# Performance work log

Measured on AMD Instinct MI355X. Metric: run time of the kernel, lower is better.

## Reference

```python
import jax, jax.numpy as jnp
import numpy as np

HIDDEN = 2048
HEADS = 16
HEAD_DIM = HIDDEN // HEADS  # 128
NUM_LATENTS = 16
LN_EPS = 1e-5


def setup_inputs() -> dict:
    key = jax.random.key(0)
    ks = jax.random.split(key, 16)
    B, S, D = 8, 4096, HIDDEN
    glorot = lambda k, fi, fo: jax.random.uniform(k, (fi, fo), jnp.float32,
                                                  -np.sqrt(6.0 / (fi + fo)), np.sqrt(6.0 / (fi + fo)))
    return {
        "hidden_states": jax.random.normal(ks[0], (B, S, D), jnp.float32),
        "ln_g": jnp.ones((D,), jnp.float32),
        "ln_b": jnp.zeros((D,), jnp.float32),
        "latents": 0.02 * jax.random.normal(ks[1], (NUM_LATENTS, D), jnp.float32),
        # weights stored as [in, out] (transpose of torch Linear.weight)
        "w_lq": glorot(ks[2], D, D), "b_lq": jnp.zeros((D,), jnp.float32),
        "w_k": glorot(ks[3], D, D), "b_k": jnp.zeros((D,), jnp.float32),
        "w_v": glorot(ks[4], D, D), "b_v": jnp.zeros((D,), jnp.float32),
        "w_lv": glorot(ks[5], D, D), "b_lv": jnp.zeros((D,), jnp.float32),
        "w_out": glorot(ks[6], D, D), "b_out": jnp.zeros((D,), jnp.float32),
    }


def reference(hidden_states, ln_g, ln_b, latents, w_lq, b_lq, w_k, b_k,
              w_v, b_v, w_lv, b_lv, w_out, b_out):
    x = hidden_states
    B, S, D = x.shape
    H, hd, L = HEADS, HEAD_DIM, latents.shape[0]
    # pre-LayerNorm
    mu = jnp.mean(x, axis=-1, keepdims=True)
    var = jnp.var(x, axis=-1, keepdims=True)
    h = (x - mu) / jnp.sqrt(var + LN_EPS) * ln_g + ln_b
    # projections
    k = (h @ w_k + b_k).reshape(B, S, H, hd)          # keys   [B,S,H,hd]
    v = (h @ w_v + b_v).reshape(B, S, H, hd)          # values [B,S,H,hd]
    q = (latents @ w_lq + b_lq).reshape(L, H, hd)     # latent queries [L,H,hd]
    # latent cross-attention: scores [B,H,L,S]
    scores = jnp.einsum("lhd,bshd->bhls", q, k) / np.sqrt(hd).astype(x.dtype)
    probs = jax.nn.softmax(scores, axis=-1)           # dropout is identity at eval
    ctx = jnp.einsum("bhls,bshd->blhd", probs, v).reshape(B, L, D)
    lv = ctx @ w_lv + b_lv                            # [B,L,D]
    pooled = jnp.mean(lv, axis=1, keepdims=True)      # [B,1,D]
    out = pooled @ w_out + b_out                      # [B,1,D]
    return x + jnp.broadcast_to(out, (B, S, D))       # residual add
```

## Files before the change

kernel.cpp:

```cpp
#include <hip/hip_runtime.h>
#include <hip/hip_bf16.h>

#define BB 8
#define SS 4096
#define DD 2048
#define HH 16
#define HDIM 128
#define LL 16
#define JJ 256
#define ROWS (BB*SS)
#define LN_EPS 1e-5f

typedef __attribute__((ext_vector_type(8))) short short8;
typedef __attribute__((ext_vector_type(4))) float f32x4;

typedef __attribute__((address_space(1))) const unsigned int gu32;
typedef __attribute__((address_space(3))) unsigned int lu32;
__device__ __forceinline__ void async16(const void* g, void* l) {
  __builtin_amdgcn_global_load_lds((gu32*)g, (lu32*)l, 16, 0, 0);
}

__device__ __forceinline__ unsigned short f2bf(float f) {
  unsigned int u = __builtin_bit_cast(unsigned int, f);
  u += 0x7fffu + ((u >> 16) & 1u);
  return (unsigned short)(u >> 16);
}
__device__ __forceinline__ float bf2f(unsigned short u) {
  unsigned int v = ((unsigned int)u) << 16;
  return __builtin_bit_cast(float, v);
}

__global__ __launch_bounds__(256) void k_q_part(const float* latents, const float* w_lq, float* qpart) {
  int c  = blockIdx.x * 256 + threadIdx.x;
  int e0 = blockIdx.y * 64;
  float acc[16];
#pragma unroll
  for (int l = 0; l < 16; ++l) acc[l] = 0.f;
  for (int e = e0; e < e0 + 64; ++e) {
    float w = w_lq[(size_t)e * 2048 + c];
#pragma unroll
    for (int l = 0; l < 16; ++l) acc[l] += latents[l * 2048 + e] * w;
  }
#pragma unroll
  for (int l = 0; l < 16; ++l) qpart[((size_t)blockIdx.y * 16 + l) * 2048 + c] = acc[l];
}

__global__ __launch_bounds__(256) void k_reduce(const float* part, const float* bias, float* out, int R) {
  int c = blockIdx.x * 256 + threadIdx.x;
  int r = blockIdx.y;
  float s = bias[c];
  for (int p = 0; p < 32; ++p) s += part[((size_t)p * R + r) * 2048 + c];
  out[r * 2048 + c] = s;
}

__global__ __launch_bounds__(256) void k_lnT(const float* x, const float* ln_g, const float* ln_b,
                                             short* h) {
  int row = blockIdx.x;
  int t = threadIdx.x;
  const float4* xr = (const float4*)(x + (size_t)row * 2048);
  float4 v0 = xr[t * 2];
  float4 v1 = xr[t * 2 + 1];
  float s  = v0.x + v0.y + v0.z + v0.w + v1.x + v1.y + v1.z + v1.w;
  float s2 = v0.x*v0.x + v0.y*v0.y + v0.z*v0.z + v0.w*v0.w
           + v1.x*v1.x + v1.y*v1.y + v1.z*v1.z + v1.w*v1.w;
#pragma unroll
  for (int o = 32; o; o >>= 1) { s += __shfl_down(s, o); s2 += __shfl_down(s2, o); }
  __shared__ float red[8];
  int wid = t >> 6;
  if ((t & 63) == 0) { red[wid] = s; red[4 + wid] = s2; }
  __syncthreads();
  float ts  = red[0] + red[1] + red[2] + red[3];
  float ts2 = red[4] + red[5] + red[6] + red[7];
  float mu   = ts * (1.0f / 2048.0f);
  float var  = ts2 * (1.0f / 2048.0f) - mu * mu;
  float rstd = rsqrtf(var + LN_EPS);
  const float4* gp = (const float4*)ln_g;
  const float4* bp = (const float4*)ln_b;
  float4 g0 = gp[t * 2], g1 = gp[t * 2 + 1];
  float4 b0 = bp[t * 2], b1 = bp[t * 2 + 1];
  short8 o;
  o[0] = (short)f2bf((v0.x - mu) * rstd * g0.x + b0.x);
  o[1] = (short)f2bf((v0.y - mu) * rstd * g0.y + b0.y);
  o[2] = (short)f2bf((v0.z - mu) * rstd * g0.z + b0.z);
  o[3] = (short)f2bf((v0.w - mu) * rstd * g0.w + b0.w);
  o[4] = (short)f2bf((v1.x - mu) * rstd * g1.x + b1.x);
  o[5] = (short)f2bf((v1.y - mu) * rstd * g1.y + b1.y);
  o[6] = (short)f2bf((v1.z - mu) * rstd * g1.z + b1.z);
  o[7] = (short)f2bf((v1.w - mu) * rstd * g1.w + b1.w);
  ((short8*)(h + (size_t)row * 2048))[t] = o;
}

__global__ __launch_bounds__(256) void k_wq(const float* w_k, const float* q, short* wq_t) {
  int e = blockIdx.x;
  __shared__ float wrow[2048];
  for (int i = threadIdx.x; i < 512; i += 256)
    ((float4*)wrow)[i] = ((const float4*)(w_k + (size_t)e * 2048))[i];
  __syncthreads();
  int j = threadIdx.x;
  int h = j >> 4, l = j & 15;
  const float* qrow = q + l * 2048 + h * 128;
  const float* wr = wrow + h * 128;
  float acc = 0.f;
#pragma unroll 8
  for (int d = 0; d < 128; ++d) acc += wr[d] * qrow[d];
  wq_t[(size_t)j * 2048 + e] = (short)f2bf(acc * 0.08838834764831845f);
}

__global__ __launch_bounds__(256, 2) void k_scores(const short* h, const short* wq_t,
                                                   short* scores, float* part_ms) {
  int s0 = blockIdx.x * 256;
  int j0 = blockIdx.y * 64;
  int b  = blockIdx.z;
  __shared__ short lds[2 * 4096 + 2 * 16384];
  int t = threadIdx.x, lane = t & 63, w = t >> 6;
  f32x4 zero = {0.f, 0.f, 0.f, 0.f};
  f32x4 acc[4][4];
#pragma unroll
  for (int m = 0; m < 4; ++m)
#pragma unroll
    for (int n = 0; n < 4; ++n) acc[m][n] = zero;

  int rsel = t >> 3;
  int kcs  = (t & 7) ^ ((t >> 3) & 7);
  const short* hbase  = h + ((size_t)(b * 4096 + s0)) * 2048;
  const short* wqbase = wq_t + (size_t)j0 * 2048;
  int koff0 = (((lane >> 4)) ^ (lane & 7)) * 8;
  int koff1 = ((4 + (lane >> 4)) ^ (lane & 7)) * 8;

  int cur = 0;
  {
    short* lA = lds;
    short* lB = lds + 8192;
#pragma unroll
    for (int i = 0; i < 8; ++i)
      async16(hbase + (size_t)(i * 32 + rsel) * 2048 + kcs * 8,
              lB + (i * 256 + w * 64) * 8);
#pragma unroll
    for (int i = 0; i < 2; ++i)
      async16(wqbase + (size_t)(i * 32 + rsel) * 2048 + kcs * 8,
              lA + (i * 256 + w * 64) * 8);
  }

  for (int it = 0; it < 32; ++it) {
    if (it < 31) {
      int k0 = (it + 1) * 64;
      short* lA1 = lds + (cur ^ 1) * 4096;
      short* lB1 = lds + 8192 + (cur ^ 1) * 16384;
#pragma unroll
      for (int i = 0; i < 8; ++i)
        async16(hbase + (size_t)(i * 32 + rsel) * 2048 + k0 + kcs * 8,
                lB1 + (i * 256 + w * 64) * 8);
#pragma unroll
      for (int i = 0; i < 2; ++i)
        async16(wqbase + (size_t)(i * 32 + rsel) * 2048 + k0 + kcs * 8,
                lA1 + (i * 256 + w * 64) * 8);
      asm volatile("s_waitcnt vmcnt(10)" ::: "memory");
    } else {
      asm volatile("s_waitcnt vmcnt(0)" ::: "memory");
    }
    __builtin_amdgcn_s_barrier();
    __builtin_amdgcn_sched_barrier(0);
    const short* lA = lds + cur * 4096;
    const short* lB = lds + 8192 + cur * 16384;
#pragma unroll
    for (int kk = 0; kk < 2; ++kk) {
      int ko = kk ? koff1 : koff0;
      short8 afr[4];
#pragma unroll
      for (int m = 0; m < 4; ++m)
        afr[m] = *(const short8*)(lA + (m * 16 + (lane & 15)) * 64 + ko);
#pragma unroll
      for (int n = 0; n < 4; ++n) {
        short8 bfr = *(const short8*)(lB + (w * 64 + n * 16 + (lane & 15)) * 64 + ko);
#pragma unroll
        for (int m = 0; m < 4; ++m)
          acc[m][n] = __builtin_amdgcn_mfma_f32_16x16x32_bf16(afr[m], bfr, acc[m][n], 0, 0, 0);
      }
    }
    __builtin_amdgcn_s_barrier();
    cur ^= 1;
  }

  int hi = lane >> 4, cc = lane & 15;
  __syncthreads();
  float2* msred = (float2*)lds;
#pragma unroll
  for (int m = 0; m < 4; ++m) {
#pragma unroll
    for (int i = 0; i < 4; ++i) {
      int j = j0 + m * 16 + hi * 4 + i;
      float v[4];
#pragma unroll
      for (int n = 0; n < 4; ++n) {
        unsigned short u = f2bf(acc[m][n][i]);
        scores[((size_t)(b * 256 + j)) * 4096 + s0 + w * 64 + n * 16 + cc] = (short)u;
        v[n] = bf2f(u);
      }
      float mx = fmaxf(fmaxf(v[0], v[1]), fmaxf(v[2], v[3]));
#pragma unroll
      for (int o = 1; o < 16; o <<= 1) mx = fmaxf(mx, __shfl_xor(mx, o));
      float sm = __expf(v[0] - mx) + __expf(v[1] - mx) + __expf(v[2] - mx) + __expf(v[3] - mx);
#pragma unroll
      for (int o = 1; o < 16; o <<= 1) sm += __shfl_xor(sm, o);
      if (cc == 0) msred[(m * 16 + hi * 4 + i) * 4 + w] = make_float2(mx, sm);
    }
  }
  __syncthreads();
  if (t < 64) {
    float2 p0 = msred[t * 4 + 0], p1 = msred[t * 4 + 1];
    float2 p2 = msred[t * 4 + 2], p3 = msred[t * 4 + 3];
    float M = fmaxf(fmaxf(p0.x, p1.x), fmaxf(p2.x, p3.x));
    float S = p0.y * __expf(p0.x - M) + p1.y * __expf(p1.x - M)
            + p2.y * __expf(p2.x - M) + p3.y * __expf(p3.x - M);
    ((float2*)part_ms)[((size_t)(b * 256 + j0 + t)) * 16 + blockIdx.x] = make_float2(M, S);
  }
}

__global__ __launch_bounds__(256) void k_pt(const short* scores, const float* part_ms,
                                            const short* h, float* Tpart) {
  int sp = blockIdx.x;
  int b  = blockIdx.y;
  int t  = threadIdx.x;
  __shared__ short sc[256 * 128];
  __shared__ float lp[16 * 128];
  __shared__ float lms[512];
  {
    const float2* p = ((const float2*)part_ms) + (size_t)(b * 256 + t) * 16;
    float2 v[16];
    float M = -1e30f;
#pragma unroll
    for (int i = 0; i < 16; ++i) { v[i] = p[i]; M = fmaxf(M, v[i].x); }
    float S = 0.f;
#pragma unroll
    for (int i = 0; i < 16; ++i) S += v[i].y * __expf(v[i].x - M);
    lms[t * 2] = M; lms[t * 2 + 1] = 1.0f / (16.0f * S);
  }
#pragma unroll
  for (int rr = 0; rr < 2; ++rr) {
    int j = rr * 128 + (t >> 1);
    const short8* src = (const short8*)(scores + ((size_t)(b * 256 + j)) * 4096 + sp * 128 + (t & 1) * 64);
    short8* dst = (short8*)(sc + j * 128 + (t & 1) * 64);
#pragma unroll
    for (int i = 0; i < 8; ++i) dst[i] = src[i];
  }
  __syncthreads();
  {
    int s = t & 127, hg = (t >> 7) * 8;
    for (int hh = hg; hh < hg + 8; ++hh) {
      float accp = 0.f;
#pragma unroll
      for (int l = 0; l < 16; ++l) {
        int r = hh * 16 + l;
        accp += __expf(bf2f((unsigned short)sc[r * 128 + s]) - lms[r * 2]) * lms[r * 2 + 1];
      }
      lp[hh * 128 + s] = accp;
    }
  }
  __syncthreads();
  f32x4 a0[16], a1[16];
#pragma unroll
  for (int hh = 0; hh < 16; ++hh) { a0[hh] = (f32x4){0,0,0,0}; a1[hh] = (f32x4){0,0,0,0}; }
  const short* hb = h + ((size_t)(b * 4096 + sp * 128)) * 2048 + t * 8;
  for (int si = 0; si < 128; ++si) {
    short8 hv8 = *(const short8*)(hb + (size_t)si * 2048);
    float hv[8];
#pragma unroll
    for (int c = 0; c < 8; ++c) hv[c] = bf2f((unsigned short)hv8[c]);
#pragma unroll
    for (int hh = 0; hh < 16; ++hh) {
      float p = lp[hh * 128 + si];
#pragma unroll
      for (int c = 0; c < 4; ++c) { a0[hh][c] += p * hv[c]; a1[hh][c] += p * hv[4 + c]; }
    }
  }
#pragma unroll
  for (int hh = 0; hh < 16; ++hh) {
    float* dst = Tpart + ((size_t)(sp * 128 + b * 16 + hh)) * 2048 + t * 8;
    *(f32x4*)dst = a0[hh];
    *(f32x4*)(dst + 4) = a1[hh];
  }
}

__global__ __launch_bounds__(256) void k_cbar_part(const float* Tpart, const float* w_v, float* part) {
  int t  = threadIdx.x;
  int c  = blockIdx.x * 256 + t;
  int e0 = blockIdx.y * 64;
  __shared__ float tb[2][8][64];
  {
    int idx = t * 4;
    int hl = idx >> 9, b = (idx >> 6) & 7, ee = idx & 63;
    int hg = blockIdx.x * 2 + hl;
    f32x4 s = {0.f, 0.f, 0.f, 0.f};
    for (int sp = 0; sp < 32; ++sp) {
      f32x4 v = *(const f32x4*)(Tpart + ((size_t)(sp * 128 + b * 16 + hg)) * 2048 + e0 + ee);
      s += v;
    }
    *(f32x4*)&tb[hl][b][ee] = s;
  }
  __syncthreads();
  int h1 = t >> 7;
  float acc[8];
#pragma unroll
  for (int b = 0; b < 8; ++b) acc[b] = 0.f;
  for (int e = 0; e < 64; ++e) {
    float wv = w_v[(size_t)(e0 + e) * 2048 + c];
#pragma unroll
    for (int b = 0; b < 8; ++b) acc[b] += tb[h1][b][e] * wv;
  }
#pragma unroll
  for (int b = 0; b < 8; ++b) part[((size_t)blockIdx.y * 8 + b) * 2048 + c] = acc[b];
}

__global__ __launch_bounds__(256) void k_vecmat_part(const float* partin, const float* bias,
                                                     const float* W, float* partout) {
  int t  = threadIdx.x;
  int c  = blockIdx.x * 256 + t;
  int e0 = blockIdx.y * 64;
  __shared__ float vin[8][64];
  {
#pragma unroll
    for (int k = 0; k < 2; ++k) {
      int idx = t * 2 + k;
      int b = idx >> 6, ee = idx & 63;
      float s = bias[e0 + ee];
      for (int p = 0; p < 32; ++p) s += partin[((size_t)p * 8 + b) * 2048 + e0 + ee];
      vin[b][ee] = s;
    }
  }
  __syncthreads();
  float acc[8];
#pragma unroll
  for (int b = 0; b < 8; ++b) acc[b] = 0.f;
  for (int e = 0; e < 64; ++e) {
    float wv = W[(size_t)(e0 + e) * 2048 + c];
#pragma unroll
    for (int b = 0; b < 8; ++b) acc[b] += vin[b][e] * wv;
  }
#pragma unroll
  for (int b = 0; b < 8; ++b) partout[((size_t)blockIdx.y * 8 + b) * 2048 + c] = acc[b];
}

__global__ __launch_bounds__(256) void k_resid(const float* x, const float* outv, float* out) {
  size_t i4 = (size_t)blockIdx.x * 256 + threadIdx.x;
  size_t total4 = (size_t)ROWS * 512;
  size_t stride = (size_t)gridDim.x * 256;
  for (; i4 < total4; i4 += stride) {
    int b  = (int)(i4 >> 21);
    int c4 = (int)(i4 & 511);
    float4 xv = ((const float4*)x)[i4];
    float4 ov = ((const float4*)outv)[b * 512 + c4];
    float4 o;
    o.x = xv.x + ov.x; o.y = xv.y + ov.y;
    o.z = xv.z + ov.z; o.w = xv.w + ov.w;
    ((float4*)out)[i4] = o;
  }
}

extern "C" void kernel_launch(void* const* d_in, const int* in_sizes, int n_in,
                              void* d_out, int out_size, void* d_ws, size_t ws_size,
                              hipStream_t stream) {
  const float* x       = (const float*)d_in[0];
  const float* ln_g    = (const float*)d_in[1];
  const float* ln_b    = (const float*)d_in[2];
  const float* latents = (const float*)d_in[3];
  const float* w_lq    = (const float*)d_in[4];
  const float* b_lq    = (const float*)d_in[5];
  const float* w_k     = (const float*)d_in[6];
  const float* w_v     = (const float*)d_in[8];
  const float* b_v     = (const float*)d_in[9];
  const float* w_lv    = (const float*)d_in[10];
  const float* b_lv    = (const float*)d_in[11];
  const float* w_out   = (const float*)d_in[12];
  const float* b_out   = (const float*)d_in[13];

  char* base = (char*)d_out;
  short* scores  = (short*)(base);
  short* h       = (short*)(base + 16777216);
  float* Tpart   = (float*)(base + 150994944);
  float* part_ms = (float*)(base + 184549376);
  float* q       = (float*)(base + 184811520);
  short* wq_t    = (short*)(base + 184942592);
  float* qpart   = (float*)(base + 185991168);
  float* part    = (float*)(base + 190185472);
  float* part2   = (float*)(base + 192282624);
  float* outv    = (float*)d_ws;
  float* out     = (float*)d_out;

  k_q_part     <<<dim3(8, 32), 256, 0, stream>>>(latents, w_lq, qpart);
  k_reduce     <<<dim3(8, 16), 256, 0, stream>>>(qpart, b_lq, q, 16);
  k_lnT        <<<32768, 256, 0, stream>>>(x, ln_g, ln_b, h);
  k_wq         <<<2048, 256, 0, stream>>>(w_k, q, wq_t);
  k_scores     <<<dim3(16, 4, 8), 256, 0, stream>>>(h, wq_t, scores, part_ms);
  k_pt         <<<dim3(32, 8), 256, 0, stream>>>(scores, part_ms, h, Tpart);
  k_cbar_part  <<<dim3(8, 32), 256, 0, stream>>>(Tpart, w_v, part);
  k_vecmat_part<<<dim3(8, 32), 256, 0, stream>>>(part, b_v, w_lv, part2);
  k_vecmat_part<<<dim3(8, 32), 256, 0, stream>>>(part2, b_lv, w_out, part);
  k_reduce     <<<dim3(8, 8), 256, 0, stream>>>(part, b_out, outv, 8);
  k_resid      <<<2048, 256, 0, stream>>>(x, outv, out);
}
```

Measured before the change: 429.3 us.

## Halve score tile width, triple-buffer loads, and split k_pt across feature halves

Measured after the change: 421.3 us, median of 2. Within noise of the previous version (-1.9%).

```diff
diff --git a/kernel.cpp b/kernel.cpp
--- a/kernel.cpp
+++ b/kernel.cpp
@@ -108,17 +108,17 @@
 
 __global__ __launch_bounds__(256, 2) void k_scores(const short* h, const short* wq_t,
                                                    short* scores, float* part_ms) {
-  int s0 = blockIdx.x * 256;
+  int s0 = blockIdx.x * 128;
   int j0 = blockIdx.y * 64;
   int b  = blockIdx.z;
-  __shared__ short lds[2 * 4096 + 2 * 16384];
+  __shared__ short lds[3 * 12288];
   int t = threadIdx.x, lane = t & 63, w = t >> 6;
   f32x4 zero = {0.f, 0.f, 0.f, 0.f};
-  f32x4 acc[4][4];
+  f32x4 acc[4][2];
 #pragma unroll
   for (int m = 0; m < 4; ++m)
 #pragma unroll
-    for (int n = 0; n < 4; ++n) acc[m][n] = zero;
+    for (int n = 0; n < 2; ++n) acc[m][n] = zero;
 
   int rsel = t >> 3;
   int kcs  = (t & 7) ^ ((t >> 3) & 7);
@@ -127,41 +127,34 @@
   int koff0 = (((lane >> 4)) ^ (lane & 7)) * 8;
   int koff1 = ((4 + (lane >> 4)) ^ (lane & 7)) * 8;
 
-  int cur = 0;
-  {
-    short* lA = lds;
-    short* lB = lds + 8192;
-#pragma unroll
-    for (int i = 0; i < 8; ++i)
-      async16(hbase + (size_t)(i * 32 + rsel) * 2048 + kcs * 8,
-              lB + (i * 256 + w * 64) * 8);
-#pragma unroll
-    for (int i = 0; i < 2; ++i)
-      async16(wqbase + (size_t)(i * 32 + rsel) * 2048 + kcs * 8,
-              lA + (i * 256 + w * 64) * 8);
-  }
-
+#define STAGE_SC(IT, BUF) { \
+    int k0_ = (IT) * 64; \
+    short* lA_ = lds + (BUF) * 12288; \
+    short* lB_ = lA_ + 4096; \
+    _Pragma("unroll") \
+    for (int i_ = 0; i_ < 4; ++i_) \
+      async16(hbase + (size_t)(i_ * 32 + rsel) * 2048 + k0_ + kcs * 8, lB_ + (i_ * 256 + t) * 8); \
+    _Pragma("unroll") \
+    for (int i_ = 0; i_ < 2; ++i_) \
+      async16(wqbase + (size_t)(i_ * 32 + rsel) * 2048 + k0_ + kcs * 8, lA_ + (i_ * 256 + t) * 8); \
+  }
+
+  STAGE_SC(0, 0);
+  STAGE_SC(1, 1);
+  int cb = 0, sb = 2;
   for (int it = 0; it < 32; ++it) {
-    if (it < 31) {
-      int k0 = (it + 1) * 64;
-      short* lA1 = lds + (cur ^ 1) * 4096;
-      short* lB1 = lds + 8192 + (cur ^ 1) * 16384;
-#pragma unroll
-      for (int i = 0; i < 8; ++i)
-        async16(hbase + (size_t)(i * 32 + rsel) * 2048 + k0 + kcs * 8,
-                lB1 + (i * 256 + w * 64) * 8);
-#pragma unroll
-      for (int i = 0; i < 2; ++i)
-        async16(wqbase + (size_t)(i * 32 + rsel) * 2048 + k0 + kcs * 8,
-                lA1 + (i * 256 + w * 64) * 8);
-      asm volatile("s_waitcnt vmcnt(10)" ::: "memory");
+    if (it < 30) {
+      STAGE_SC(it + 2, sb);
+      asm volatile("s_waitcnt vmcnt(12)" ::: "memory");
+    } else if (it == 30) {
+      asm volatile("s_waitcnt vmcnt(6)" ::: "memory");
     } else {
       asm volatile("s_waitcnt vmcnt(0)" ::: "memory");
     }
     __builtin_amdgcn_s_barrier();
     __builtin_amdgcn_sched_barrier(0);
-    const short* lA = lds + cur * 4096;
-    const short* lB = lds + 8192 + cur * 16384;
+    const short* lA = lds + cb * 12288;
+    const short* lB = lA + 4096;
 #pragma unroll
     for (int kk = 0; kk < 2; ++kk) {
       int ko = kk ? koff1 : koff0;
@@ -170,16 +163,18 @@
       for (int m = 0; m < 4; ++m)
         afr[m] = *(const short8*)(lA + (m * 16 + (lane & 15)) * 64 + ko);
 #pragma unroll
-      for (int n = 0; n < 4; ++n) {
-        short8 bfr = *(const short8*)(lB + (w * 64 + n * 16 + (lane & 15)) * 64 + ko);
+      for (int n = 0; n < 2; ++n) {
+        short8 bfr = *(const short8*)(lB + (w * 32 + n * 16 + (lane & 15)) * 64 + ko);
 #pragma unroll
         for (int m = 0; m < 4; ++m)
           acc[m][n] = __builtin_amdgcn_mfma_f32_16x16x32_bf16(afr[m], bfr, acc[m][n], 0, 0, 0);
       }
     }
     __builtin_amdgcn_s_barrier();
-    cur ^= 1;
-  }
+    cb = (cb == 2) ? 0 : cb + 1;
+    sb = (sb == 2) ? 0 : sb + 1;
+  }
+#undef STAGE_SC
 
   int hi = lane >> 4, cc = lane & 15;
   __syncthreads();
@@ -189,17 +184,17 @@
 #pragma unroll
     for (int i = 0; i < 4; ++i) {
       int j = j0 + m * 16 + hi * 4 + i;
-      float v[4];
-#pragma unroll
-      for (int n = 0; n < 4; ++n) {
+      float v[2];
+#pragma unroll
+      for (int n = 0; n < 2; ++n) {
         unsigned short u = f2bf(acc[m][n][i]);
-        scores[((size_t)(b * 256 + j)) * 4096 + s0 + w * 64 + n * 16 + cc] = (short)u;
+        scores[((size_t)(b * 256 + j)) * 4096 + s0 + w * 32 + n * 16 + cc] = (short)u;
         v[n] = bf2f(u);
       }
-      float mx = fmaxf(fmaxf(v[0], v[1]), fmaxf(v[2], v[3]));
+      float mx = fmaxf(v[0], v[1]);
 #pragma unroll
       for (int o = 1; o < 16; o <<= 1) mx = fmaxf(mx, __shfl_xor(mx, o));
-      float sm = __expf(v[0] - mx) + __expf(v[1] - mx) + __expf(v[2] - mx) + __expf(v[3] - mx);
+      float sm = __expf(v[0] - mx) + __expf(v[1] - mx);
 #pragma unroll
       for (int o = 1; o < 16; o <<= 1) sm += __shfl_xor(sm, o);
       if (cc == 0) msred[(m * 16 + hi * 4 + i) * 4 + w] = make_float2(mx, sm);
@@ -212,7 +207,7 @@
     float M = fmaxf(fmaxf(p0.x, p1.x), fmaxf(p2.x, p3.x));
     float S = p0.y * __expf(p0.x - M) + p1.y * __expf(p1.x - M)
             + p2.y * __expf(p2.x - M) + p3.y * __expf(p3.x - M);
-    ((float2*)part_ms)[((size_t)(b * 256 + j0 + t)) * 16 + blockIdx.x] = make_float2(M, S);
+    ((float2*)part_ms)[((size_t)(b * 256 + j0 + t)) * 32 + blockIdx.x] = make_float2(M, S);
   }
 }
 
@@ -220,19 +215,19 @@
                                             const short* h, float* Tpart) {
   int sp = blockIdx.x;
   int b  = blockIdx.y;
+  int eh = blockIdx.z;
   int t  = threadIdx.x;
   __shared__ short sc[256 * 128];
   __shared__ float lp[16 * 128];
   __shared__ float lms[512];
   {
-    const float2* p = ((const float2*)part_ms) + (size_t)(b * 256 + t) * 16;
-    float2 v[16];
+    const float2* p = ((const float2*)part_ms) + (size_t)(b * 256 + t) * 32;
     float M = -1e30f;
 #pragma unroll
-    for (int i = 0; i < 16; ++i) { v[i] = p[i]; M = fmaxf(M, v[i].x); }
+    for (int i = 0; i < 32; ++i) M = fmaxf(M, p[i].x);
     float S = 0.f;
 #pragma unroll
-    for (int i = 0; i < 16; ++i) S += v[i].y * __expf(v[i].x - M);
+    for (int i = 0; i < 32; ++i) S += p[i].y * __expf(p[i].x - M);
     lms[t * 2] = M; lms[t * 2 + 1] = 1.0f / (16.0f * S);
   }
 #pragma unroll
@@ -257,28 +252,26 @@
     }
   }
   __syncthreads();
-  f32x4 a0[16], a1[16];
-#pragma unroll
-  for (int hh = 0; hh < 16; ++hh) { a0[hh] = (f32x4){0,0,0,0}; a1[hh] = (f32x4){0,0,0,0}; }
-  const short* hb = h + ((size_t)(b * 4096 + sp * 128)) * 2048 + t * 8;
+  f32x4 a[16];
+#pragma unroll
+  for (int hh = 0; hh < 16; ++hh) a[hh] = (f32x4){0.f, 0.f, 0.f, 0.f};
+  int e0 = eh * 1024 + t * 4;
+  const short* hb = h + ((size_t)(b * 4096 + sp * 128)) * 2048 + e0;
   for (int si = 0; si < 128; ++si) {
-    short8 hv8 = *(const short8*)(hb + (size_t)si * 2048);
-    float hv[8];
-#pragma unroll
-    for (int c = 0; c < 8; ++c) hv[c] = bf2f((unsigned short)hv8[c]);
+    short4 hv4 = *(const short4*)(hb + (size_t)si * 2048);
+    float hv[4];
+    hv[0] = bf2f((unsigned short)hv4.x); hv[1] = bf2f((unsigned short)hv4.y);
+    hv[2] = bf2f((unsigned short)hv4.z); hv[3] = bf2f((unsigned short)hv4.w);
 #pragma unroll
     for (int hh = 0; hh < 16; ++hh) {
       float p = lp[hh * 128 + si];
 #pragma unroll
-      for (int c = 0; c < 4; ++c) { a0[hh][c] += p * hv[c]; a1[hh][c] += p * hv[4 + c]; }
-    }
-  }
-#pragma unroll
-  for (int hh = 0; hh < 16; ++hh) {
-    float* dst = Tpart + ((size_t)(sp * 128 + b * 16 + hh)) * 2048 + t * 8;
-    *(f32x4*)dst = a0[hh];
-    *(f32x4*)(dst + 4) = a1[hh];
-  }
+      for (int c = 0; c < 4; ++c) a[hh][c] += p * hv[c];
+    }
+  }
+#pragma unroll
+  for (int hh = 0; hh < 16; ++hh)
+    *(f32x4*)(Tpart + ((size_t)(sp * 128 + b * 16 + hh)) * 2048 + e0) = a[hh];
 }
 
 __global__ __launch_bounds__(256) void k_cbar_part(const float* Tpart, const float* w_v, float* part) {
@@ -378,11 +371,11 @@
   short* h       = (short*)(base + 16777216);
   float* Tpart   = (float*)(base + 150994944);
   float* part_ms = (float*)(base + 184549376);
-  float* q       = (float*)(base + 184811520);
-  short* wq_t    = (short*)(base + 184942592);
-  float* qpart   = (float*)(base + 185991168);
-  float* part    = (float*)(base + 190185472);
-  float* part2   = (float*)(base + 192282624);
+  float* q       = (float*)(base + 185073664);
+  short* wq_t    = (short*)(base + 185204736);
+  float* qpart   = (float*)(base + 186253312);
+  float* part    = (float*)(base + 190447616);
+  float* part2   = (float*)(base + 192544768);
   float* outv    = (float*)d_ws;
   float* out     = (float*)d_out;
 
@@ -390,8 +383,8 @@
   k_reduce     <<<dim3(8, 16), 256, 0, stream>>>(qpart, b_lq, q, 16);
   k_lnT        <<<32768, 256, 0, stream>>>(x, ln_g, ln_b, h);
   k_wq         <<<2048, 256, 0, stream>>>(w_k, q, wq_t);
-  k_scores     <<<dim3(16, 4, 8), 256, 0, stream>>>(h, wq_t, scores, part_ms);
-  k_pt         <<<dim3(32, 8), 256, 0, stream>>>(scores, part_ms, h, Tpart);
+  k_scores     <<<dim3(32, 4, 8), 256, 0, stream>>>(h, wq_t, scores, part_ms);
+  k_pt         <<<dim3(32, 8, 2), 256, 0, stream>>>(scores, part_ms, h, Tpart);
   k_cbar_part  <<<dim3(8, 32), 256, 0, stream>>>(Tpart, w_v, part);
   k_vecmat_part<<<dim3(8, 32), 256, 0, stream>>>(part, b_v, w_lv, part2);
   k_vecmat_part<<<dim3(8, 32), 256, 0, stream>>>(part2, b_lv, w_out, part);
```

## Retile scores GEMM over all 256 query columns and split PT across feature halves

Applied to the files above, without the earlier changes.

New measurement: 424.7 us. No clear change (-1.1%).

```diff
diff --git a/kernel.cpp b/kernel.cpp
--- a/kernel.cpp
+++ b/kernel.cpp
@@ -108,10 +108,9 @@
 
 __global__ __launch_bounds__(256, 2) void k_scores(const short* h, const short* wq_t,
                                                    short* scores, float* part_ms) {
-  int s0 = blockIdx.x * 256;
-  int j0 = blockIdx.y * 64;
-  int b  = blockIdx.z;
-  __shared__ short lds[2 * 4096 + 2 * 16384];
+  int s0 = blockIdx.x * 64;
+  int b  = blockIdx.y;
+  __shared__ short lds[2 * 16384 + 2 * 4096];
   int t = threadIdx.x, lane = t & 63, w = t >> 6;
   f32x4 zero = {0.f, 0.f, 0.f, 0.f};
   f32x4 acc[4][4];
@@ -120,58 +119,57 @@
 #pragma unroll
     for (int n = 0; n < 4; ++n) acc[m][n] = zero;
 
-  int rsel = t >> 3;
-  int kcs  = (t & 7) ^ ((t >> 3) & 7);
-  const short* hbase  = h + ((size_t)(b * 4096 + s0)) * 2048;
-  const short* wqbase = wq_t + (size_t)j0 * 2048;
+  int jlo = w * 8 + (lane >> 3);
+  int kcs = (lane & 7) ^ ((lane >> 3) & 7);
+  const short* hbase = h + ((size_t)(b * 4096 + s0)) * 2048;
   int koff0 = (((lane >> 4)) ^ (lane & 7)) * 8;
   int koff1 = ((4 + (lane >> 4)) ^ (lane & 7)) * 8;
 
   int cur = 0;
   {
     short* lA = lds;
-    short* lB = lds + 8192;
+    short* lB = lds + 32768;
 #pragma unroll
     for (int i = 0; i < 8; ++i)
-      async16(hbase + (size_t)(i * 32 + rsel) * 2048 + kcs * 8,
+      async16(wq_t + (size_t)(i * 32 + jlo) * 2048 + kcs * 8,
+              lA + (i * 256 + w * 64) * 8);
+#pragma unroll
+    for (int i = 0; i < 2; ++i)
+      async16(hbase + (size_t)(i * 32 + jlo) * 2048 + kcs * 8,
               lB + (i * 256 + w * 64) * 8);
-#pragma unroll
-    for (int i = 0; i < 2; ++i)
-      async16(wqbase + (size_t)(i * 32 + rsel) * 2048 + kcs * 8,
-              lA + (i * 256 + w * 64) * 8);
   }
 
   for (int it = 0; it < 32; ++it) {
     if (it < 31) {
       int k0 = (it + 1) * 64;
-      short* lA1 = lds + (cur ^ 1) * 4096;
-      short* lB1 = lds + 8192 + (cur ^ 1) * 16384;
+      short* lA1 = lds + (cur ^ 1) * 16384;
+      short* lB1 = lds + 32768 + (cur ^ 1) * 4096;
 #pragma unroll
       for (int i = 0; i < 8; ++i)
-        async16(hbase + (size_t)(i * 32 + rsel) * 2048 + k0 + kcs * 8,
+        async16(wq_t + (size_t)(i * 32 + jlo) * 2048 + k0 + kcs * 8,
+                lA1 + (i * 256 + w * 64) * 8);
+#pragma unroll
+      for (int i = 0; i < 2; ++i)
+        async16(hbase + (size_t)(i * 32 + jlo) * 2048 + k0 + kcs * 8,
                 lB1 + (i * 256 + w * 64) * 8);
-#pragma unroll
-      for (int i = 0; i < 2; ++i)
-        async16(wqbase + (size_t)(i * 32 + rsel) * 2048 + k0 + kcs * 8,
-                lA1 + (i * 256 + w * 64) * 8);
       asm volatile("s_waitcnt vmcnt(10)" ::: "memory");
     } else {
       asm volatile("s_waitcnt vmcnt(0)" ::: "memory");
     }
     __builtin_amdgcn_s_barrier();
     __builtin_amdgcn_sched_barrier(0);
-    const short* lA = lds + cur * 4096;
-    const short* lB = lds + 8192 + cur * 16384;
+    const short* lA = lds + cur * 16384;
+    const short* lB = lds + 32768 + cur * 4096;
 #pragma unroll
     for (int kk = 0; kk < 2; ++kk) {
       int ko = kk ? koff1 : koff0;
       short8 afr[4];
 #pragma unroll
       for (int m = 0; m < 4; ++m)
-        afr[m] = *(const short8*)(lA + (m * 16 + (lane & 15)) * 64 + ko);
+        afr[m] = *(const short8*)(lA + (w * 64 + m * 16 + (lane & 15)) * 64 + ko);
 #pragma unroll
       for (int n = 0; n < 4; ++n) {
-        short8 bfr = *(const short8*)(lB + (w * 64 + n * 16 + (lane & 15)) * 64 + ko);
+        short8 bfr = *(const short8*)(lB + (n * 16 + (lane & 15)) * 64 + ko);
 #pragma unroll
         for (int m = 0; m < 4; ++m)
           acc[m][n] = __builtin_amdgcn_mfma_f32_16x16x32_bf16(afr[m], bfr, acc[m][n], 0, 0, 0);
@@ -182,18 +180,16 @@
   }
 
   int hi = lane >> 4, cc = lane & 15;
-  __syncthreads();
-  float2* msred = (float2*)lds;
 #pragma unroll
   for (int m = 0; m < 4; ++m) {
 #pragma unroll
     for (int i = 0; i < 4; ++i) {
-      int j = j0 + m * 16 + hi * 4 + i;
+      int j = w * 64 + m * 16 + hi * 4 + i;
       float v[4];
 #pragma unroll
       for (int n = 0; n < 4; ++n) {
         unsigned short u = f2bf(acc[m][n][i]);
-        scores[((size_t)(b * 256 + j)) * 4096 + s0 + w * 64 + n * 16 + cc] = (short)u;
+        scores[((size_t)(b * 256 + j)) * 4096 + s0 + n * 16 + cc] = (short)u;
         v[n] = bf2f(u);
       }
       float mx = fmaxf(fmaxf(v[0], v[1]), fmaxf(v[2], v[3]));
@@ -202,17 +198,9 @@
       float sm = __expf(v[0] - mx) + __expf(v[1] - mx) + __expf(v[2] - mx) + __expf(v[3] - mx);
 #pragma unroll
       for (int o = 1; o < 16; o <<= 1) sm += __shfl_xor(sm, o);
-      if (cc == 0) msred[(m * 16 + hi * 4 + i) * 4 + w] = make_float2(mx, sm);
-    }
-  }
-  __syncthreads();
-  if (t < 64) {
-    float2 p0 = msred[t * 4 + 0], p1 = msred[t * 4 + 1];
-    float2 p2 = msred[t * 4 + 2], p3 = msred[t * 4 + 3];
-    float M = fmaxf(fmaxf(p0.x, p1.x), fmaxf(p2.x, p3.x));
-    float S = p0.y * __expf(p0.x - M) + p1.y * __expf(p1.x - M)
-            + p2.y * __expf(p2.x - M) + p3.y * __expf(p3.x - M);
-    ((float2*)part_ms)[((size_t)(b * 256 + j0 + t)) * 16 + blockIdx.x] = make_float2(M, S);
+      if (cc == 0)
+        ((float2*)part_ms)[((size_t)(b * 256 + j)) * 64 + blockIdx.x] = make_float2(mx, sm);
+    }
   }
 }
 
@@ -220,19 +208,19 @@
                                             const short* h, float* Tpart) {
   int sp = blockIdx.x;
   int b  = blockIdx.y;
+  int eh = blockIdx.z;
   int t  = threadIdx.x;
   __shared__ short sc[256 * 128];
   __shared__ float lp[16 * 128];
   __shared__ float lms[512];
   {
-    const float2* p = ((const float2*)part_ms) + (size_t)(b * 256 + t) * 16;
-    float2 v[16];
+    const float2* p = ((const float2*)part_ms) + (size_t)(b * 256 + t) * 64;
     float M = -1e30f;
-#pragma unroll
-    for (int i = 0; i < 16; ++i) { v[i] = p[i]; M = fmaxf(M, v[i].x); }
+#pragma unroll 8
+    for (int i = 0; i < 64; ++i) M = fmaxf(M, p[i].x);
     float S = 0.f;
-#pragma unroll
-    for (int i = 0; i < 16; ++i) S += v[i].y * __expf(v[i].x - M);
+#pragma unroll 8
+    for (int i = 0; i < 64; ++i) S += p[i].y * __expf(p[i].x - M);
     lms[t * 2] = M; lms[t * 2 + 1] = 1.0f / (16.0f * S);
   }
 #pragma unroll
@@ -257,28 +245,26 @@
     }
   }
   __syncthreads();
-  f32x4 a0[16], a1[16];
-#pragma unroll
-  for (int hh = 0; hh < 16; ++hh) { a0[hh] = (f32x4){0,0,0,0}; a1[hh] = (f32x4){0,0,0,0}; }
-  const short* hb = h + ((size_t)(b * 4096 + sp * 128)) * 2048 + t * 8;
+  f32x4 a[16];
+#pragma unroll
+  for (int hh = 0; hh < 16; ++hh) a[hh] = (f32x4){0.f, 0.f, 0.f, 0.f};
+  int e0 = eh * 1024 + t * 4;
+  const short* hb = h + ((size_t)(b * 4096 + sp * 128)) * 2048 + e0;
   for (int si = 0; si < 128; ++si) {
-    short8 hv8 = *(const short8*)(hb + (size_t)si * 2048);
-    float hv[8];
-#pragma unroll
-    for (int c = 0; c < 8; ++c) hv[c] = bf2f((unsigned short)hv8[c]);
+    short4 hv4 = *(const short4*)(hb + (size_t)si * 2048);
+    float hv[4];
+    hv[0] = bf2f((unsigned short)hv4.x); hv[1] = bf2f((unsigned short)hv4.y);
+    hv[2] = bf2f((unsigned short)hv4.z); hv[3] = bf2f((unsigned short)hv4.w);
 #pragma unroll
     for (int hh = 0; hh < 16; ++hh) {
       float p = lp[hh * 128 + si];
 #pragma unroll
-      for (int c = 0; c < 4; ++c) { a0[hh][c] += p * hv[c]; a1[hh][c] += p * hv[4 + c]; }
-    }
-  }
-#pragma unroll
-  for (int hh = 0; hh < 16; ++hh) {
-    float* dst = Tpart + ((size_t)(sp * 128 + b * 16 + hh)) * 2048 + t * 8;
-    *(f32x4*)dst = a0[hh];
-    *(f32x4*)(dst + 4) = a1[hh];
-  }
+      for (int c = 0; c < 4; ++c) a[hh][c] += p * hv[c];
+    }
+  }
+#pragma unroll
+  for (int hh = 0; hh < 16; ++hh)
+    *(f32x4*)(Tpart + ((size_t)(sp * 128 + b * 16 + hh)) * 2048 + e0) = a[hh];
 }
 
 __global__ __launch_bounds__(256) void k_cbar_part(const float* Tpart, const float* w_v, float* part) {
@@ -378,11 +364,11 @@
   short* h       = (short*)(base + 16777216);
   float* Tpart   = (float*)(base + 150994944);
   float* part_ms = (float*)(base + 184549376);
-  float* q       = (float*)(base + 184811520);
-  short* wq_t    = (short*)(base + 184942592);
-  float* qpart   = (float*)(base + 185991168);
-  float* part    = (float*)(base + 190185472);
-  float* part2   = (float*)(base + 192282624);
+  float* q       = (float*)(base + 185597952);
+  short* wq_t    = (short*)(base + 185729024);
+  float* qpart   = (float*)(base + 186777600);
+  float* part    = (float*)(base + 190971904);
+  float* part2   = (float*)(base + 193069056);
   float* outv    = (float*)d_ws;
   float* out     = (float*)d_out;
 
@@ -390,8 +376,8 @@
   k_reduce     <<<dim3(8, 16), 256, 0, stream>>>(qpart, b_lq, q, 16);
   k_lnT        <<<32768, 256, 0, stream>>>(x, ln_g, ln_b, h);
   k_wq         <<<2048, 256, 0, stream>>>(w_k, q, wq_t);
-  k_scores     <<<dim3(16, 4, 8), 256, 0, stream>>>(h, wq_t, scores, part_ms);
-  k_pt         <<<dim3(32, 8), 256, 0, stream>>>(scores, part_ms, h, Tpart);
+  k_scores     <<<dim3(64, 8), 256, 0, stream>>>(h, wq_t, scores, part_ms);
+  k_pt         <<<dim3(32, 8, 2), 256, 0, stream>>>(scores, part_ms, h, Tpart);
   k_cbar_part  <<<dim3(8, 32), 256, 0, stream>>>(Tpart, w_v, part);
   k_vecmat_part<<<dim3(8, 32), 256, 0, stream>>>(part, b_v, w_lv, part2);
   k_vecmat_part<<<dim3(8, 32), 256, 0, stream>>>(part2, b_lv, w_out, part);
```
